# Kernel tuning notes

Hardware: AMD Instinct MI355X
Metric: run time of the kernel (lower is better)

The kernel has to match this reference:

```python
import jax, jax.numpy as jnp
import numpy as np

NODELEN = 394
N_NODES = 50000
N_EDGES = 200000
IN_DIM = 2 * NODELEN  # 788
H2 = 192
EMB = 128


def setup_inputs() -> dict:
    key = jax.random.key(0)
    ks = jax.random.split(key, 12)
    inp = {
        'features': jax.random.normal(ks[0], (N_NODES, NODELEN), dtype=jnp.float32),
        'src': jax.random.randint(ks[1], (N_EDGES,), 0, N_NODES),
        'dst': jax.random.randint(ks[2], (N_EDGES,), 0, N_NODES),
        # AutoEncoder params (Linear weights stored as [in, out])
        'W_enc1': jax.random.normal(ks[3], (IN_DIM, H2), dtype=jnp.float32) / np.sqrt(IN_DIM),
        'b_enc1': jnp.zeros((H2,), dtype=jnp.float32),
        'W_enc3': jax.random.normal(ks[4], (H2, EMB), dtype=jnp.float32) / np.sqrt(H2),
        'b_enc3': jnp.zeros((EMB,), dtype=jnp.float32),
        'W_dec1': jax.random.normal(ks[5], (EMB, H2), dtype=jnp.float32) / np.sqrt(EMB),
        'b_dec1': jnp.zeros((H2,), dtype=jnp.float32),
        'W_dec3': jax.random.normal(ks[6], (H2, IN_DIM), dtype=jnp.float32) / np.sqrt(H2),
        'b_dec3': jnp.zeros((IN_DIM,), dtype=jnp.float32),
    }
    return inp


def _segment_mean(msgs, dst, inv_deg, n):
    # msgs: [E, F] gathered neighbor features; mean over incoming edges per node
    return jax.ops.segment_sum(msgs, dst, num_segments=n) * inv_deg


def reference(features, src, dst, W_enc1, b_enc1, W_enc3, b_enc3,
              W_dec1, b_dec1, W_dec3, b_dec3):
    n = features.shape[0]
    ones = jnp.ones(src.shape[0], dtype=features.dtype)
    deg = jax.ops.segment_sum(ones, dst, num_segments=n)
    # nodes with no neighbors fall back to the zero dummy vector (as in source)
    inv_deg = (1.0 / jnp.maximum(deg, 1.0))[:, None]

    # depth-1 aggregation: mean of raw neighbor features, then feat[0] := 0
    h1 = _segment_mean(features[src], dst, inv_deg, n)
    h1 = h1.at[:, 0].set(0.0)
    # depth-2 aggregation: mean of depth-1 aggregates of neighbors, feat[0] := 0
    h2 = _segment_mean(h1[src], dst, inv_deg, n)
    h2 = h2.at[:, 0].set(0.0)

    # concatenated embedding with positions 0 and NODELEN zeroed
    emb = jnp.concatenate([features, h2], axis=1)  # [N, 788]
    emb = emb.at[:, 0].set(0.0).at[:, NODELEN].set(0.0)

    # AutoEncoder forward (dropout is identity at inference)
    x = jax.nn.relu(emb @ W_enc1 + b_enc1)
    encoded = x @ W_enc3 + b_enc3
    y = jax.nn.relu(encoded @ W_dec1 + b_dec1)
    decoded = y @ W_dec3 + b_dec3
    return encoded, decoded, emb
```

## Files before the change

### kernel.cpp

```cpp
#include <hip/hip_runtime.h>
#include <hip/hip_bf16.h>

#define NODELEN 394
#define IN_DIM 788
#define H2DIM 192
#define EMBDIM 128
#define NCHUNK 197

typedef __attribute__((ext_vector_type(4))) float f32x4;
typedef __attribute__((ext_vector_type(8))) short bfrag;

static __device__ __forceinline__ unsigned short f2bf(float f) {
    union { float f; unsigned u; } v; v.f = f;
    unsigned r = v.u + 0x7FFFu + ((v.u >> 16) & 1u);
    return (unsigned short)(r >> 16);
}
static __device__ __forceinline__ float bf2f(unsigned short h) {
    union { unsigned u; float f; } v; v.u = ((unsigned)h) << 16;
    return v.f;
}


__global__ void count_deg(const int* __restrict__ dst, int* __restrict__ deg, int e) {
    int i = blockIdx.x * blockDim.x + threadIdx.x;
    if (i < e) atomicAdd(&deg[dst[i]], 1);
}

__global__ void block_sum(const int* __restrict__ deg, int* __restrict__ bsum, int n) {
    __shared__ int s[256];
    int t = threadIdx.x;
    int i = blockIdx.x * 256 + t;
    s[t] = (i < n) ? deg[i] : 0;
    __syncthreads();
    for (int d = 128; d > 0; d >>= 1) {
        if (t < d) s[t] += s[t + d];
        __syncthreads();
    }
    if (t == 0) bsum[blockIdx.x] = s[0];
}

__global__ void scan_bsums(int* bsum, int nb) {
    __shared__ int s[256];
    int t = threadIdx.x;
    int x0 = (t < nb) ? bsum[t] : 0;
    s[t] = x0;
    __syncthreads();
    for (int d = 1; d < 256; d <<= 1) {
        int u = (t >= d) ? s[t - d] : 0;
        __syncthreads();
        s[t] += u;
        __syncthreads();
    }
    if (t < nb) bsum[t] = s[t] - x0;
}

__global__ void block_scan(const int* __restrict__ deg, const int* __restrict__ boff,
                           int* __restrict__ rowstart, int* __restrict__ cursor,
                           float* __restrict__ inv, int n) {
    __shared__ int s[256];
    int t = threadIdx.x;
    int i = blockIdx.x * 256 + t;
    int x0 = (i < n) ? deg[i] : 0;
    s[t] = x0;
    __syncthreads();
    for (int d = 1; d < 256; d <<= 1) {
        int u = (t >= d) ? s[t - d] : 0;
        __syncthreads();
        s[t] += u;
        __syncthreads();
    }
    if (i < n) {
        int r = boff[blockIdx.x] + s[t] - x0;
        rowstart[i] = r;
        cursor[i] = r;
        inv[i] = 1.0f / fmaxf((float)x0, 1.0f);
    }
}

__global__ void fill_edges(const int* __restrict__ src, const int* __restrict__ dst,
                           int* __restrict__ cursor, int* __restrict__ elist, int e) {
    int i = blockIdx.x * blockDim.x + threadIdx.x;
    if (i < e) {
        int p = atomicAdd(&cursor[dst[i]], 1);
        elist[p] = src[i];
    }
}


__global__ __launch_bounds__(256) void gather1(
        const float* __restrict__ feat, const int* __restrict__ rowstart,
        const int* __restrict__ deg, const float* __restrict__ inv,
        const int* __restrict__ elist, unsigned short* __restrict__ h1) {
    const int node = blockIdx.x;
    const int c = threadIdx.x;
    if (c >= NCHUNK) return;
    const int beg = rowstart[node];
    const int dc = deg[node];
    const float s = inv[node];
    const size_t off = (size_t)c * 2;

    float ax = 0.f, ay = 0.f, bx = 0.f, by = 0.f;
    float cx = 0.f, cy = 0.f, dx = 0.f, dy = 0.f;
    int j = 0;
    for (; j + 3 < dc; j += 4) {
        int n0 = elist[beg + j], n1 = elist[beg + j + 1];
        int n2 = elist[beg + j + 2], n3 = elist[beg + j + 3];
        float2 v0 = *(const float2*)(feat + (size_t)n0 * NODELEN + off);
        float2 v1 = *(const float2*)(feat + (size_t)n1 * NODELEN + off);
        float2 v2 = *(const float2*)(feat + (size_t)n2 * NODELEN + off);
        float2 v3 = *(const float2*)(feat + (size_t)n3 * NODELEN + off);
        ax += v0.x; ay += v0.y; bx += v1.x; by += v1.y;
        cx += v2.x; cy += v2.y; dx += v3.x; dy += v3.y;
    }
    for (; j < dc; ++j) {
        int n0 = elist[beg + j];
        float2 v0 = *(const float2*)(feat + (size_t)n0 * NODELEN + off);
        ax += v0.x; ay += v0.y;
    }
    float fx = (ax + bx + cx + dx) * s;
    float fy = (ay + by + cy + dy) * s;
    if (c == 0) fx = 0.f;
    unsigned out = ((unsigned)f2bf(fy) << 16) | (unsigned)f2bf(fx);
    *(unsigned*)(h1 + (size_t)node * NODELEN + off) = out;
}

__global__ __launch_bounds__(256) void gather2_emb(
        const float* __restrict__ feat, const unsigned* __restrict__ h1,
        const int* __restrict__ rowstart, const int* __restrict__ deg,
        const float* __restrict__ inv, const int* __restrict__ elist,
        float* __restrict__ emb) {
    const int node = blockIdx.x;
    const int c = threadIdx.x;
    if (c >= NCHUNK) return;
    const int beg = rowstart[node];
    const int dc = deg[node];
    const float s = inv[node];

    float ax = 0.f, ay = 0.f, bx = 0.f, by = 0.f;
    float cx = 0.f, cy = 0.f, dx = 0.f, dy = 0.f;
    int j = 0;
    for (; j + 3 < dc; j += 4) {
        int n0 = elist[beg + j], n1 = elist[beg + j + 1];
        int n2 = elist[beg + j + 2], n3 = elist[beg + j + 3];
        unsigned u0 = h1[(size_t)n0 * NCHUNK + c];
        unsigned u1 = h1[(size_t)n1 * NCHUNK + c];
        unsigned u2 = h1[(size_t)n2 * NCHUNK + c];
        unsigned u3 = h1[(size_t)n3 * NCHUNK + c];
        ax += bf2f((unsigned short)u0); ay += bf2f((unsigned short)(u0 >> 16));
        bx += bf2f((unsigned short)u1); by += bf2f((unsigned short)(u1 >> 16));
        cx += bf2f((unsigned short)u2); cy += bf2f((unsigned short)(u2 >> 16));
        dx += bf2f((unsigned short)u3); dy += bf2f((unsigned short)(u3 >> 16));
    }
    for (; j < dc; ++j) {
        int n0 = elist[beg + j];
        unsigned u0 = h1[(size_t)n0 * NCHUNK + c];
        ax += bf2f((unsigned short)u0); ay += bf2f((unsigned short)(u0 >> 16));
    }
    float hx = (ax + bx + cx + dx) * s;
    float hy = (ay + by + cy + dy) * s;

    const float* fr = feat + (size_t)node * NODELEN;
    float* er = emb + (size_t)node * IN_DIM;
    float2 fv = *(const float2*)(fr + c * 2);
    if (c == 0) { fv.x = 0.f; hx = 0.f; }
    *(float2*)(er + c * 2) = fv;
    float2 hv; hv.x = hx; hv.y = hy;
    *(float2*)(er + NODELEN + c * 2) = hv;
}

__device__ __forceinline__ void tr_one(const float* W, unsigned short* Wt,
                                       int K, int N, int Kp, int idx) {
    int nrow = idx / Kp, k = idx - nrow * Kp;
    Wt[idx] = (k < K) ? f2bf(W[(size_t)k * N + nrow]) : (unsigned short)0;
}

#define T1E (192 * 800)
#define T2E (128 * 192)
#define T3E (192 * 128)
#define T4E (788 * 192)

__global__ void transpose_all(const float* __restrict__ W1, unsigned short* __restrict__ Wt1,
                              const float* __restrict__ W2, unsigned short* __restrict__ Wt2,
                              const float* __restrict__ W3, unsigned short* __restrict__ Wt3,
                              const float* __restrict__ W4, unsigned short* __restrict__ Wt4) {
    int idx = blockIdx.x * 256 + threadIdx.x;
    if (idx < T1E) { tr_one(W1, Wt1, IN_DIM, H2DIM, 800, idx); return; }
    idx -= T1E;
    if (idx < T2E) { tr_one(W2, Wt2, H2DIM, EMBDIM, 192, idx); return; }
    idx -= T2E;
    if (idx < T3E) { tr_one(W3, Wt3, EMBDIM, H2DIM, 128, idx); return; }
    idx -= T3E;
    if (idx < T4E) { tr_one(W4, Wt4, H2DIM, IN_DIM, 192, idx); return; }
}

static __device__ __forceinline__ int bs_addr(int r, int s) {
    return r * 32 + ((s ^ ((r >> 1) & 3)) << 3);
}
static __device__ __forceinline__ int xy_base(int r, int s) {
    int ph = (s & 24) | ((s ^ r) & 7);
    return r * 192 + (ph << 3);
}
static __device__ __forceinline__ int xy_addr_s(int r, int col) { return xy_base(r, col >> 3) + (col & 7); }

static __device__ __forceinline__ unsigned short f2bf_fast(float f) {
    __hip_bfloat16 h = __float2bfloat16(f);
    union { __hip_bfloat16 h; unsigned short u; } c; c.h = h; return c.u;
}

struct A8 { float4 a, b; };

static __device__ __forceinline__ void load_a(A8 out[2], const float* __restrict__ emb,
                                              int m0, int wm, int lr, int lk, int M, int kt) {
    int c = kt * 32 + lk * 8;
    #pragma unroll
    for (int i = 0; i < 2; ++i) {
        int gm = m0 + wm * 32 + i * 16 + lr;
        const float* rp = emb + (size_t)gm * IN_DIM;
        bool v = gm < M;
        if (v && c + 8 <= IN_DIM) {
            out[i].a = *(const float4*)(rp + c);
            out[i].b = *(const float4*)(rp + c + 4);
        } else {
            float t[8];
            #pragma unroll
            for (int q = 0; q < 8; ++q) t[q] = (v && c + q < IN_DIM) ? rp[c + q] : 0.f;
            out[i].a = make_float4(t[0], t[1], t[2], t[3]);
            out[i].b = make_float4(t[4], t[5], t[6], t[7]);
        }
    }
}

static __device__ __forceinline__ bfrag cvt_a(const A8& x) {
    union { unsigned short u[8]; bfrag v; } pk;
    pk.u[0] = f2bf_fast(x.a.x); pk.u[1] = f2bf_fast(x.a.y);
    pk.u[2] = f2bf_fast(x.a.z); pk.u[3] = f2bf_fast(x.a.w);
    pk.u[4] = f2bf_fast(x.b.x); pk.u[5] = f2bf_fast(x.b.y);
    pk.u[6] = f2bf_fast(x.b.z); pk.u[7] = f2bf_fast(x.b.w);
    return pk.v;
}

__global__ __launch_bounds__(256, 3) void mlp12(
    const float* __restrict__ emb,
    const unsigned short* __restrict__ Wt1,
    const unsigned short* __restrict__ Wt2,
    const float* __restrict__ b1, const float* __restrict__ b2,
    float* __restrict__ encoded, unsigned short* __restrict__ enc16, int M)
{
    __shared__ unsigned short XY[64 * 192];
    __shared__ unsigned short Bs[2][192 * 32];

    const int tid = threadIdx.x;
    const int wid = tid >> 6, l = tid & 63;
    const int wm = wid >> 1, wn = wid & 1;
    const int lr = l & 15, lk = l >> 4;
    const int m0 = blockIdx.x * 64;

    const int r0 = tid >> 2, s0 = tid & 3;
    const int r1 = (tid + 256) >> 2;
    const int r2 = (tid + 512) >> 2;
    const int bw0 = bs_addr(r0, s0);
    const int bw1 = bs_addr(r1, s0);
    const int bw2 = bs_addr(r2, s0);
    int brd6[6], brd4[4];
    #pragma unroll
    for (int j = 0; j < 6; ++j) brd6[j] = bs_addr(wn * 96 + j * 16 + lr, lk);
    #pragma unroll
    for (int j = 0; j < 4; ++j) brd4[j] = bs_addr(wn * 64 + j * 16 + lr, lk);

    {
        f32x4 acc[2][6];
        #pragma unroll
        for (int i = 0; i < 2; ++i)
            #pragma unroll
            for (int j = 0; j < 6; ++j) acc[i][j] = (f32x4){0.f, 0.f, 0.f, 0.f};

        A8 aC[2], aN[2];
        bfrag bC[3], bN[3];
        load_a(aC, emb, m0, wm, lr, lk, M, 0);
        bC[0] = *(const bfrag*)(Wt1 + (size_t)r0 * 800 + s0 * 8);
        bC[1] = *(const bfrag*)(Wt1 + (size_t)r1 * 800 + s0 * 8);
        bC[2] = *(const bfrag*)(Wt1 + (size_t)r2 * 800 + s0 * 8);

        #pragma unroll 5
        for (int kt = 0; kt < 25; ++kt) {
            unsigned short* B = Bs[kt & 1];
            *(bfrag*)&B[bw0] = bC[0];
            *(bfrag*)&B[bw1] = bC[1];
            *(bfrag*)&B[bw2] = bC[2];
            if (kt < 24) {
                int k0 = (kt + 1) * 32;
                load_a(aN, emb, m0, wm, lr, lk, M, kt + 1);
                bN[0] = *(const bfrag*)(Wt1 + (size_t)r0 * 800 + k0 + s0 * 8);
                bN[1] = *(const bfrag*)(Wt1 + (size_t)r1 * 800 + k0 + s0 * 8);
                bN[2] = *(const bfrag*)(Wt1 + (size_t)r2 * 800 + k0 + s0 * 8);
            }
            __syncthreads();
            bfrag af0 = cvt_a(aC[0]), af1 = cvt_a(aC[1]);
            bfrag bf[6];
            #pragma unroll
            for (int j = 0; j < 6; ++j) bf[j] = *(const bfrag*)&B[brd6[j]];
            #pragma unroll
            for (int j = 0; j < 6; ++j) {
                acc[0][j] = __builtin_amdgcn_mfma_f32_16x16x32_bf16(af0, bf[j], acc[0][j], 0, 0, 0);
                acc[1][j] = __builtin_amdgcn_mfma_f32_16x16x32_bf16(af1, bf[j], acc[1][j], 0, 0, 0);
            }
            if (kt < 24) {
                aC[0] = aN[0]; aC[1] = aN[1];
                bC[0] = bN[0]; bC[1] = bN[1]; bC[2] = bN[2];
            }
        }
        float bv[6];
        #pragma unroll
        for (int j = 0; j < 6; ++j) bv[j] = b1[wn * 96 + j * 16 + lr];
        #pragma unroll
        for (int i = 0; i < 2; ++i)
            #pragma unroll
            for (int j = 0; j < 6; ++j)
                #pragma unroll
                for (int r = 0; r < 4; ++r) {
                    int m = wm * 32 + i * 16 + lk * 4 + r;
                    int n1 = wn * 96 + j * 16 + lr;
                    XY[xy_addr_s(m, n1)] = f2bf_fast(fmaxf(acc[i][j][r] + bv[j], 0.f));
                }
    }
    __syncthreads();

    {
        bfrag af2[6][2];
        #pragma unroll
        for (int q = 0; q < 6; ++q)
            #pragma unroll
            for (int i = 0; i < 2; ++i)
                af2[q][i] = *(const bfrag*)&XY[xy_base(wm * 32 + i * 16 + lr, q * 4 + lk)];

        f32x4 acc[2][4];
        #pragma unroll
        for (int i = 0; i < 2; ++i)
            #pragma unroll
            for (int j = 0; j < 4; ++j) acc[i][j] = (f32x4){0.f, 0.f, 0.f, 0.f};

        bfrag bC[2], bN[2];
        bC[0] = *(const bfrag*)(Wt2 + (size_t)r0 * 192 + s0 * 8);
        bC[1] = *(const bfrag*)(Wt2 + (size_t)r1 * 192 + s0 * 8);

        #pragma unroll
        for (int kt = 0; kt < 6; ++kt) {
            unsigned short* B = Bs[kt & 1];
            *(bfrag*)&B[bw0] = bC[0];
            *(bfrag*)&B[bw1] = bC[1];
            if (kt < 5) {
                int k0 = (kt + 1) * 32;
                bN[0] = *(const bfrag*)(Wt2 + (size_t)r0 * 192 + k0 + s0 * 8);
                bN[1] = *(const bfrag*)(Wt2 + (size_t)r1 * 192 + k0 + s0 * 8);
            }
            __syncthreads();
            bfrag bf[4];
            #pragma unroll
            for (int j = 0; j < 4; ++j) bf[j] = *(const bfrag*)&B[brd4[j]];
            #pragma unroll
            for (int i = 0; i < 2; ++i)
                #pragma unroll
                for (int j = 0; j < 4; ++j)
                    acc[i][j] = __builtin_amdgcn_mfma_f32_16x16x32_bf16(af2[kt][i], bf[j], acc[i][j], 0, 0, 0);
            if (kt < 5) { bC[0] = bN[0]; bC[1] = bN[1]; }
        }

        float bv[4];
        #pragma unroll
        for (int j = 0; j < 4; ++j) bv[j] = b2[wn * 64 + j * 16 + lr];
        #pragma unroll
        for (int i = 0; i < 2; ++i)
            #pragma unroll
            for (int j = 0; j < 4; ++j)
                #pragma unroll
                for (int r = 0; r < 4; ++r) {
                    int m = wm * 32 + i * 16 + lk * 4 + r;
                    int nn = wn * 64 + j * 16 + lr;
                    float v = acc[i][j][r] + bv[j];
                    int gm = m0 + m;
                    if (gm < M) {
                        encoded[(size_t)gm * EMBDIM + nn] = v;
                        enc16[(size_t)gm * EMBDIM + nn] = f2bf_fast(v);
                    }
                }
    }
}

__global__ __launch_bounds__(256, 3) void mlp34(
    const unsigned short* __restrict__ enc16,
    const unsigned short* __restrict__ Wt3,
    const unsigned short* __restrict__ Wt4,
    const float* __restrict__ b3, const float* __restrict__ b4,
    float* __restrict__ decoded, int M)
{
    __shared__ unsigned short XY[64 * 192];
    __shared__ unsigned short Bs[2][192 * 32];

    const int tid = threadIdx.x;
    const int wid = tid >> 6, l = tid & 63;
    const int wm = wid >> 1, wn = wid & 1;
    const int lr = l & 15, lk = l >> 4;
    const int m0 = blockIdx.x * 64;
    const bfrag zf = {0, 0, 0, 0, 0, 0, 0, 0};

    const int r0 = tid >> 2, s0 = tid & 3;
    const int r1 = (tid + 256) >> 2;
    const int r2 = (tid + 512) >> 2;
    const int bw0 = bs_addr(r0, s0);
    const int bw1 = bs_addr(r1, s0);
    const int bw2 = bs_addr(r2, s0);
    int brd6[6];
    #pragma unroll
    for (int j = 0; j < 6; ++j) brd6[j] = bs_addr(wn * 96 + j * 16 + lr, lk);

    {
        bfrag af3[4][2];
        #pragma unroll
        for (int q = 0; q < 4; ++q)
            #pragma unroll
            for (int i = 0; i < 2; ++i) {
                int gm = m0 + wm * 32 + i * 16 + lr;
                af3[q][i] = (gm < M)
                    ? *(const bfrag*)(enc16 + (size_t)gm * EMBDIM + q * 32 + lk * 8) : zf;
            }

        f32x4 acc[2][6];
        #pragma unroll
        for (int i = 0; i < 2; ++i)
            #pragma unroll
            for (int j = 0; j < 6; ++j) acc[i][j] = (f32x4){0.f, 0.f, 0.f, 0.f};

        bfrag bC[3], bN[3];
        bC[0] = *(const bfrag*)(Wt3 + (size_t)r0 * 128 + s0 * 8);
        bC[1] = *(const bfrag*)(Wt3 + (size_t)r1 * 128 + s0 * 8);
        bC[2] = *(const bfrag*)(Wt3 + (size_t)r2 * 128 + s0 * 8);

        #pragma unroll
        for (int kt = 0; kt < 4; ++kt) {
            unsigned short* B = Bs[kt & 1];
            *(bfrag*)&B[bw0] = bC[0];
            *(bfrag*)&B[bw1] = bC[1];
            *(bfrag*)&B[bw2] = bC[2];
            if (kt < 3) {
                int k0 = (kt + 1) * 32;
                bN[0] = *(const bfrag*)(Wt3 + (size_t)r0 * 128 + k0 + s0 * 8);
                bN[1] = *(const bfrag*)(Wt3 + (size_t)r1 * 128 + k0 + s0 * 8);
                bN[2] = *(const bfrag*)(Wt3 + (size_t)r2 * 128 + k0 + s0 * 8);
            }
            __syncthreads();
            bfrag bf[6];
            #pragma unroll
            for (int j = 0; j < 6; ++j) bf[j] = *(const bfrag*)&B[brd6[j]];
            #pragma unroll
            for (int i = 0; i < 2; ++i)
                #pragma unroll
                for (int j = 0; j < 6; ++j)
                    acc[i][j] = __builtin_amdgcn_mfma_f32_16x16x32_bf16(af3[kt][i], bf[j], acc[i][j], 0, 0, 0);
            if (kt < 3) { bC[0] = bN[0]; bC[1] = bN[1]; bC[2] = bN[2]; }
        }

        float bv[6];
        #pragma unroll
        for (int j = 0; j < 6; ++j) bv[j] = b3[wn * 96 + j * 16 + lr];
        #pragma unroll
        for (int i = 0; i < 2; ++i)
            #pragma unroll
            for (int j = 0; j < 6; ++j)
                #pragma unroll
                for (int r = 0; r < 4; ++r) {
                    int m = wm * 32 + i * 16 + lk * 4 + r;
                    int nc = wn * 96 + j * 16 + lr;
                    XY[xy_addr_s(m, nc)] = f2bf_fast(fmaxf(acc[i][j][r] + bv[j], 0.f));
                }
    }
    __syncthreads();

    {
        bfrag af4[6][2];
        #pragma unroll
        for (int q = 0; q < 6; ++q)
            #pragma unroll
            for (int i = 0; i < 2; ++i)
                af4[q][i] = *(const bfrag*)&XY[xy_base(wm * 32 + i * 16 + lr, q * 4 + lk)];

        bfrag bC[3], bN[3];
        bC[0] = *(const bfrag*)(Wt4 + (size_t)r0 * 192 + s0 * 8);
        bC[1] = *(const bfrag*)(Wt4 + (size_t)r1 * 192 + s0 * 8);
        bC[2] = *(const bfrag*)(Wt4 + (size_t)r2 * 192 + s0 * 8);

        for (int nc = 0; nc < 5; ++nc) {
            f32x4 acc[2][6];
            #pragma unroll
            for (int i = 0; i < 2; ++i)
                #pragma unroll
                for (int j = 0; j < 6; ++j) acc[i][j] = (f32x4){0.f, 0.f, 0.f, 0.f};

            #pragma unroll
            for (int kt = 0; kt < 6; ++kt) {
                const int t = nc * 6 + kt;
                unsigned short* B = Bs[t & 1];
                *(bfrag*)&B[bw0] = bC[0];
                *(bfrag*)&B[bw1] = bC[1];
                *(bfrag*)&B[bw2] = bC[2];
                if (t < 29) {
                    int nn = (kt < 5) ? nc : nc + 1;
                    int nk = (kt < 5) ? (kt + 1) * 32 : 0;
                    int g0 = nn * 192 + r0, g1 = nn * 192 + r1, g2 = nn * 192 + r2;
                    bN[0] = (g0 < IN_DIM) ? *(const bfrag*)(Wt4 + (size_t)g0 * 192 + nk + s0 * 8) : zf;
                    bN[1] = (g1 < IN_DIM) ? *(const bfrag*)(Wt4 + (size_t)g1 * 192 + nk + s0 * 8) : zf;
                    bN[2] = (g2 < IN_DIM) ? *(const bfrag*)(Wt4 + (size_t)g2 * 192 + nk + s0 * 8) : zf;
                }
                __syncthreads();
                bfrag bf[6];
                #pragma unroll
                for (int j = 0; j < 6; ++j) bf[j] = *(const bfrag*)&B[brd6[j]];
                #pragma unroll
                for (int i = 0; i < 2; ++i)
                    #pragma unroll
                    for (int j = 0; j < 6; ++j)
                        acc[i][j] = __builtin_amdgcn_mfma_f32_16x16x32_bf16(af4[kt][i], bf[j], acc[i][j], 0, 0, 0);
                bC[0] = bN[0]; bC[1] = bN[1]; bC[2] = bN[2];
            }

            float bv[6];
            #pragma unroll
            for (int j = 0; j < 6; ++j) {
                int nn = nc * 192 + wn * 96 + j * 16 + lr;
                bv[j] = (nn < IN_DIM) ? b4[nn] : 0.f;
            }
            #pragma unroll
            for (int i = 0; i < 2; ++i)
                #pragma unroll
                for (int j = 0; j < 6; ++j)
                    #pragma unroll
                    for (int r = 0; r < 4; ++r) {
                        int gm = m0 + wm * 32 + i * 16 + lk * 4 + r;
                        int nn = nc * 192 + wn * 96 + j * 16 + lr;
                        if (gm < M && nn < IN_DIM)
                            decoded[(size_t)gm * IN_DIM + nn] = acc[i][j][r] + bv[j];
                    }
        }
    }
}


extern "C" void kernel_launch(void* const* d_in, const int* in_sizes, int n_in,
                              void* d_out, int out_size, void* d_ws, size_t ws_size,
                              hipStream_t stream) {
    const float* features = (const float*)d_in[0];
    const int*   src      = (const int*)d_in[1];
    const int*   dst      = (const int*)d_in[2];
    const float* W_enc1   = (const float*)d_in[3];
    const float* b_enc1   = (const float*)d_in[4];
    const float* W_enc3   = (const float*)d_in[5];
    const float* b_enc3   = (const float*)d_in[6];
    const float* W_dec1   = (const float*)d_in[7];
    const float* b_dec1   = (const float*)d_in[8];
    const float* W_dec3   = (const float*)d_in[9];
    const float* b_dec3   = (const float*)d_in[10];

    const int n = in_sizes[0] / NODELEN;
    const int e = in_sizes[1];

    float* encoded = (float*)d_out;
    float* decoded = encoded + (size_t)n * EMBDIM;
    float* emb     = decoded + (size_t)n * IN_DIM;

    char* ws = (char*)d_ws;
    unsigned short* h1    = (unsigned short*)(ws + 0);
    unsigned short* enc16 = (unsigned short*)(ws + 0);
    unsigned short* Wt1 = (unsigned short*)(ws + 40000000);
    unsigned short* Wt2 = (unsigned short*)(ws + 40400000);
    unsigned short* Wt3 = (unsigned short*)(ws + 40500000);
    unsigned short* Wt4 = (unsigned short*)(ws + 40600000);
    float* inv          = (float*)(ws + 41000000);
    int*   deg          = (int*)  (ws + 41200000);
    int*   rowstart     = (int*)  (ws + 41400000);
    int*   cursor       = (int*)  (ws + 41600000);
    int*   elist        = (int*)  (ws + 41800000);
    int*   bsum         = (int*)  (ws + 42600000);

    const int nb = (n + 255) / 256;
    const int eb = (e + 255) / 256;

    transpose_all<<<(T1E + T2E + T3E + T4E + 255) / 256, 256, 0, stream>>>(
        W_enc1, Wt1, W_enc3, Wt2, W_dec1, Wt3, W_dec3, Wt4);

    hipMemsetAsync(deg, 0, (size_t)n * sizeof(int), stream);
    count_deg<<<eb, 256, 0, stream>>>(dst, deg, e);
    block_sum<<<nb, 256, 0, stream>>>(deg, bsum, n);
    scan_bsums<<<1, 256, 0, stream>>>(bsum, nb);
    block_scan<<<nb, 256, 0, stream>>>(deg, bsum, rowstart, cursor, inv, n);
    fill_edges<<<eb, 256, 0, stream>>>(src, dst, cursor, elist, e);

    gather1<<<n, 256, 0, stream>>>(features, rowstart, deg, inv, elist, h1);
    gather2_emb<<<n, 256, 0, stream>>>(features, (const unsigned*)h1, rowstart, deg,
                                       inv, elist, emb);

    const int MB = (n + 63) / 64;
    mlp12<<<MB, 256, 0, stream>>>(emb, Wt1, Wt2, b_enc1, b_enc3, encoded, enc16, n);
    mlp34<<<MB, 256, 0, stream>>>(enc16, Wt3, Wt4, b_dec1, b_dec3, decoded, n);
}
```

Before: 350.7 us.

## Enlarge MLP row tiles to 128 and stage a bf16 copy of emb

Both MLP kernels now give each block 128 rows instead of 64, so each weight tile loaded into shared memory feeds more MFMAs. Occupancy drops to 2 blocks per CU. The double-buffered B pipeline now writes the next buffer after the MFMAs with a single barrier per step, and the decoder uses 128-column N tiles. When the workspace is large enough, gather2 also writes a padded bf16 copy of emb, so mlp12 reads half as many bytes and skips the fp32-to-bf16 conversion. The cost is an extra write pass and more register pressure.

```diff
diff --git a/kernel.cpp b/kernel.cpp
--- a/kernel.cpp
+++ b/kernel.cpp
@@ -10,6 +10,9 @@
 typedef __attribute__((ext_vector_type(4))) float f32x4;
 typedef __attribute__((ext_vector_type(8))) short bfrag;
 
+#define LBAR() do { asm volatile("s_waitcnt lgkmcnt(0)" ::: "memory"); \
+                    __builtin_amdgcn_s_barrier(); } while (0)
+
 static __device__ __forceinline__ unsigned short f2bf(float f) {
     union { float f; unsigned u; } v; v.f = f;
     unsigned r = v.u + 0x7FFFu + ((v.u >> 16) & 1u);
@@ -18,6 +21,10 @@
 static __device__ __forceinline__ float bf2f(unsigned short h) {
     union { unsigned u; float f; } v; v.u = ((unsigned)h) << 16;
     return v.f;
+}
+static __device__ __forceinline__ unsigned short f2bf_fast(float f) {
+    __hip_bfloat16 h = __float2bfloat16(f);
+    union { __hip_bfloat16 h; unsigned short u; } c; c.h = h; return c.u;
 }
 
 
@@ -128,7 +135,7 @@
         const float* __restrict__ feat, const unsigned* __restrict__ h1,
         const int* __restrict__ rowstart, const int* __restrict__ deg,
         const float* __restrict__ inv, const int* __restrict__ elist,
-        float* __restrict__ emb) {
+        float* __restrict__ emb, unsigned* __restrict__ emb16u) {
     const int node = blockIdx.x;
     const int c = threadIdx.x;
     if (c >= NCHUNK) return;
@@ -166,6 +173,13 @@
     *(float2*)(er + c * 2) = fv;
     float2 hv; hv.x = hx; hv.y = hy;
     *(float2*)(er + NODELEN + c * 2) = hv;
+
+    if (emb16u) {
+        unsigned* e16 = emb16u + (size_t)node * 400;
+        e16[c]          = ((unsigned)f2bf(fv.y) << 16) | (unsigned)f2bf(fv.x);
+        e16[NCHUNK + c] = ((unsigned)f2bf(hy)  << 16) | (unsigned)f2bf(hx);
+        if (c < 6) e16[394 + c] = 0u;
+    }
 }
 
 __device__ __forceinline__ void tr_one(const float* W, unsigned short* Wt,
@@ -202,62 +216,50 @@
 }
 static __device__ __forceinline__ int xy_addr_s(int r, int col) { return xy_base(r, col >> 3) + (col & 7); }
 
-static __device__ __forceinline__ unsigned short f2bf_fast(float f) {
-    __hip_bfloat16 h = __float2bfloat16(f);
-    union { __hip_bfloat16 h; unsigned short u; } c; c.h = h; return c.u;
-}
-
-struct A8 { float4 a, b; };
-
-static __device__ __forceinline__ void load_a(A8 out[2], const float* __restrict__ emb,
-                                              int m0, int wm, int lr, int lk, int M, int kt) {
-    int c = kt * 32 + lk * 8;
-    #pragma unroll
-    for (int i = 0; i < 2; ++i) {
-        int gm = m0 + wm * 32 + i * 16 + lr;
-        const float* rp = emb + (size_t)gm * IN_DIM;
-        bool v = gm < M;
-        if (v && c + 8 <= IN_DIM) {
-            out[i].a = *(const float4*)(rp + c);
-            out[i].b = *(const float4*)(rp + c + 4);
+static __device__ __forceinline__ bfrag load_af_bf(const unsigned short* A800, int gm, int M, int col) {
+    const bfrag zf = {0, 0, 0, 0, 0, 0, 0, 0};
+    return (gm < M) ? *(const bfrag*)(A800 + (size_t)gm * 800 + col) : zf;
+}
+static __device__ __forceinline__ bfrag load_af_f32(const float* A, int gm, int M, int col) {
+    float t[8];
+    #pragma unroll
+    for (int q = 0; q < 8; ++q) t[q] = 0.f;
+    if (gm < M) {
+        const float* rp = A + (size_t)gm * IN_DIM;
+        if (col + 8 <= IN_DIM) {
+            float4 v0 = *(const float4*)(rp + col), v1 = *(const float4*)(rp + col + 4);
+            t[0] = v0.x; t[1] = v0.y; t[2] = v0.z; t[3] = v0.w;
+            t[4] = v1.x; t[5] = v1.y; t[6] = v1.z; t[7] = v1.w;
         } else {
-            float t[8];
-            #pragma unroll
-            for (int q = 0; q < 8; ++q) t[q] = (v && c + q < IN_DIM) ? rp[c + q] : 0.f;
-            out[i].a = make_float4(t[0], t[1], t[2], t[3]);
-            out[i].b = make_float4(t[4], t[5], t[6], t[7]);
+            #pragma unroll
+            for (int q = 0; q < 8; ++q) if (col + q < IN_DIM) t[q] = rp[col + q];
         }
     }
-}
-
-static __device__ __forceinline__ bfrag cvt_a(const A8& x) {
     union { unsigned short u[8]; bfrag v; } pk;
-    pk.u[0] = f2bf_fast(x.a.x); pk.u[1] = f2bf_fast(x.a.y);
-    pk.u[2] = f2bf_fast(x.a.z); pk.u[3] = f2bf_fast(x.a.w);
-    pk.u[4] = f2bf_fast(x.b.x); pk.u[5] = f2bf_fast(x.b.y);
-    pk.u[6] = f2bf_fast(x.b.z); pk.u[7] = f2bf_fast(x.b.w);
+    #pragma unroll
+    for (int q = 0; q < 8; ++q) pk.u[q] = f2bf_fast(t[q]);
     return pk.v;
 }
 
-__global__ __launch_bounds__(256, 3) void mlp12(
-    const float* __restrict__ emb,
+template <int ABF>
+__global__ __launch_bounds__(256, 2) void mlp12(
+    const void* __restrict__ Aemb,
     const unsigned short* __restrict__ Wt1,
     const unsigned short* __restrict__ Wt2,
     const float* __restrict__ b1, const float* __restrict__ b2,
     float* __restrict__ encoded, unsigned short* __restrict__ enc16, int M)
 {
-    __shared__ unsigned short XY[64 * 192];
+    __shared__ unsigned short XY[128 * 192];
     __shared__ unsigned short Bs[2][192 * 32];
 
     const int tid = threadIdx.x;
     const int wid = tid >> 6, l = tid & 63;
     const int wm = wid >> 1, wn = wid & 1;
     const int lr = l & 15, lk = l >> 4;
-    const int m0 = blockIdx.x * 64;
+    const int m0 = blockIdx.x * 128;
 
     const int r0 = tid >> 2, s0 = tid & 3;
-    const int r1 = (tid + 256) >> 2;
-    const int r2 = (tid + 512) >> 2;
+    const int r1 = r0 + 64, r2 = r0 + 128;
     const int bw0 = bs_addr(r0, s0);
     const int bw1 = bs_addr(r1, s0);
     const int bw2 = bs_addr(r2, s0);
@@ -267,58 +269,68 @@
     #pragma unroll
     for (int j = 0; j < 4; ++j) brd4[j] = bs_addr(wn * 64 + j * 16 + lr, lk);
 
+    int gmA[4];
+    #pragma unroll
+    for (int i = 0; i < 4; ++i) gmA[i] = m0 + wm * 64 + i * 16 + lr;
+
     {
-        f32x4 acc[2][6];
-        #pragma unroll
-        for (int i = 0; i < 2; ++i)
+        f32x4 acc[4][6];
+        #pragma unroll
+        for (int i = 0; i < 4; ++i)
             #pragma unroll
             for (int j = 0; j < 6; ++j) acc[i][j] = (f32x4){0.f, 0.f, 0.f, 0.f};
 
-        A8 aC[2], aN[2];
-        bfrag bC[3], bN[3];
-        load_a(aC, emb, m0, wm, lr, lk, M, 0);
-        bC[0] = *(const bfrag*)(Wt1 + (size_t)r0 * 800 + s0 * 8);
-        bC[1] = *(const bfrag*)(Wt1 + (size_t)r1 * 800 + s0 * 8);
-        bC[2] = *(const bfrag*)(Wt1 + (size_t)r2 * 800 + s0 * 8);
+        bfrag afC[4], afN[4], bN[3];
+        #pragma unroll
+        for (int i = 0; i < 4; ++i)
+            afC[i] = ABF ? load_af_bf((const unsigned short*)Aemb, gmA[i], M, lk * 8)
+                         : load_af_f32((const float*)Aemb, gmA[i], M, lk * 8);
+        *(bfrag*)&Bs[0][bw0] = *(const bfrag*)(Wt1 + (size_t)r0 * 800 + s0 * 8);
+        *(bfrag*)&Bs[0][bw1] = *(const bfrag*)(Wt1 + (size_t)r1 * 800 + s0 * 8);
+        *(bfrag*)&Bs[0][bw2] = *(const bfrag*)(Wt1 + (size_t)r2 * 800 + s0 * 8);
+        LBAR();
 
         #pragma unroll 5
         for (int kt = 0; kt < 25; ++kt) {
-            unsigned short* B = Bs[kt & 1];
-            *(bfrag*)&B[bw0] = bC[0];
-            *(bfrag*)&B[bw1] = bC[1];
-            *(bfrag*)&B[bw2] = bC[2];
             if (kt < 24) {
                 int k0 = (kt + 1) * 32;
-                load_a(aN, emb, m0, wm, lr, lk, M, kt + 1);
+                #pragma unroll
+                for (int i = 0; i < 4; ++i)
+                    afN[i] = ABF ? load_af_bf((const unsigned short*)Aemb, gmA[i], M, k0 + lk * 8)
+                                 : load_af_f32((const float*)Aemb, gmA[i], M, k0 + lk * 8);
                 bN[0] = *(const bfrag*)(Wt1 + (size_t)r0 * 800 + k0 + s0 * 8);
                 bN[1] = *(const bfrag*)(Wt1 + (size_t)r1 * 800 + k0 + s0 * 8);
                 bN[2] = *(const bfrag*)(Wt1 + (size_t)r2 * 800 + k0 + s0 * 8);
             }
-            __syncthreads();
-            bfrag af0 = cvt_a(aC[0]), af1 = cvt_a(aC[1]);
+            const unsigned short* B = Bs[kt & 1];
             bfrag bf[6];
             #pragma unroll
             for (int j = 0; j < 6; ++j) bf[j] = *(const bfrag*)&B[brd6[j]];
             #pragma unroll
-            for (int j = 0; j < 6; ++j) {
-                acc[0][j] = __builtin_amdgcn_mfma_f32_16x16x32_bf16(af0, bf[j], acc[0][j], 0, 0, 0);
-                acc[1][j] = __builtin_amdgcn_mfma_f32_16x16x32_bf16(af1, bf[j], acc[1][j], 0, 0, 0);
-            }
+            for (int i = 0; i < 4; ++i)
+                #pragma unroll
+                for (int j = 0; j < 6; ++j)
+                    acc[i][j] = __builtin_amdgcn_mfma_f32_16x16x32_bf16(afC[i], bf[j], acc[i][j], 0, 0, 0);
             if (kt < 24) {
-                aC[0] = aN[0]; aC[1] = aN[1];
-                bC[0] = bN[0]; bC[1] = bN[1]; bC[2] = bN[2];
+                unsigned short* Bn = Bs[(kt + 1) & 1];
+                *(bfrag*)&Bn[bw0] = bN[0];
+                *(bfrag*)&Bn[bw1] = bN[1];
+                *(bfrag*)&Bn[bw2] = bN[2];
+                LBAR();
+                #pragma unroll
+                for (int i = 0; i < 4; ++i) afC[i] = afN[i];
             }
         }
         float bv[6];
         #pragma unroll
         for (int j = 0; j < 6; ++j) bv[j] = b1[wn * 96 + j * 16 + lr];
         #pragma unroll
-        for (int i = 0; i < 2; ++i)
+        for (int i = 0; i < 4; ++i)
             #pragma unroll
             for (int j = 0; j < 6; ++j)
                 #pragma unroll
                 for (int r = 0; r < 4; ++r) {
-                    int m = wm * 32 + i * 16 + lk * 4 + r;
+                    int m = wm * 64 + i * 16 + lk * 4 + r;
                     int n1 = wn * 96 + j * 16 + lr;
                     XY[xy_addr_s(m, n1)] = f2bf_fast(fmaxf(acc[i][j][r] + bv[j], 0.f));
                 }
@@ -326,55 +338,54 @@
     __syncthreads();
 
     {
-        bfrag af2[6][2];
-        #pragma unroll
-        for (int q = 0; q < 6; ++q)
-            #pragma unroll
-            for (int i = 0; i < 2; ++i)
-                af2[q][i] = *(const bfrag*)&XY[xy_base(wm * 32 + i * 16 + lr, q * 4 + lk)];
-
-        f32x4 acc[2][4];
-        #pragma unroll
-        for (int i = 0; i < 2; ++i)
+        f32x4 acc[4][4];
+        #pragma unroll
+        for (int i = 0; i < 4; ++i)
             #pragma unroll
             for (int j = 0; j < 4; ++j) acc[i][j] = (f32x4){0.f, 0.f, 0.f, 0.f};
 
-        bfrag bC[2], bN[2];
-        bC[0] = *(const bfrag*)(Wt2 + (size_t)r0 * 192 + s0 * 8);
-        bC[1] = *(const bfrag*)(Wt2 + (size_t)r1 * 192 + s0 * 8);
+        bfrag bN[2];
+        *(bfrag*)&Bs[0][bw0] = *(const bfrag*)(Wt2 + (size_t)r0 * 192 + s0 * 8);
+        *(bfrag*)&Bs[0][bw1] = *(const bfrag*)(Wt2 + (size_t)r1 * 192 + s0 * 8);
+        LBAR();
 
         #pragma unroll
         for (int kt = 0; kt < 6; ++kt) {
-            unsigned short* B = Bs[kt & 1];
-            *(bfrag*)&B[bw0] = bC[0];
-            *(bfrag*)&B[bw1] = bC[1];
             if (kt < 5) {
                 int k0 = (kt + 1) * 32;
                 bN[0] = *(const bfrag*)(Wt2 + (size_t)r0 * 192 + k0 + s0 * 8);
                 bN[1] = *(const bfrag*)(Wt2 + (size_t)r1 * 192 + k0 + s0 * 8);
             }
-            __syncthreads();
-            bfrag bf[4];
+            const unsigned short* B = Bs[kt & 1];
+            bfrag af[4], bf[4];
+            #pragma unroll
+            for (int i = 0; i < 4; ++i)
+                af[i] = *(const bfrag*)&XY[xy_base(wm * 64 + i * 16 + lr, kt * 4 + lk)];
             #pragma unroll
             for (int j = 0; j < 4; ++j) bf[j] = *(const bfrag*)&B[brd4[j]];
             #pragma unroll
-            for (int i = 0; i < 2; ++i)
+            for (int i = 0; i < 4; ++i)
                 #pragma unroll
                 for (int j = 0; j < 4; ++j)
-                    acc[i][j] = __builtin_amdgcn_mfma_f32_16x16x32_bf16(af2[kt][i], bf[j], acc[i][j], 0, 0, 0);
-            if (kt < 5) { bC[0] = bN[0]; bC[1] = bN[1]; }
+                    acc[i][j] = __builtin_amdgcn_mfma_f32_16x16x32_bf16(af[i], bf[j], acc[i][j], 0, 0, 0);
+            if (kt < 5) {
+                unsigned short* Bn = Bs[(kt + 1) & 1];
+                *(bfrag*)&Bn[bw0] = bN[0];
+                *(bfrag*)&Bn[bw1] = bN[1];
+                LBAR();
+            }
         }
 
         float bv[4];
         #pragma unroll
         for (int j = 0; j < 4; ++j) bv[j] = b2[wn * 64 + j * 16 + lr];
         #pragma unroll
-        for (int i = 0; i < 2; ++i)
+        for (int i = 0; i < 4; ++i)
             #pragma unroll
             for (int j = 0; j < 4; ++j)
                 #pragma unroll
                 for (int r = 0; r < 4; ++r) {
-                    int m = wm * 32 + i * 16 + lk * 4 + r;
+                    int m = wm * 64 + i * 16 + lk * 4 + r;
                     int nn = wn * 64 + j * 16 + lr;
                     float v = acc[i][j][r] + bv[j];
                     int gm = m0 + m;
@@ -386,89 +397,96 @@
     }
 }
 
-__global__ __launch_bounds__(256, 3) void mlp34(
+__global__ __launch_bounds__(256, 2) void mlp34(
     const unsigned short* __restrict__ enc16,
     const unsigned short* __restrict__ Wt3,
     const unsigned short* __restrict__ Wt4,
     const float* __restrict__ b3, const float* __restrict__ b4,
     float* __restrict__ decoded, int M)
 {
-    __shared__ unsigned short XY[64 * 192];
+    __shared__ unsigned short XY[128 * 192];
     __shared__ unsigned short Bs[2][192 * 32];
 
     const int tid = threadIdx.x;
     const int wid = tid >> 6, l = tid & 63;
     const int wm = wid >> 1, wn = wid & 1;
     const int lr = l & 15, lk = l >> 4;
-    const int m0 = blockIdx.x * 64;
+    const int m0 = blockIdx.x * 128;
     const bfrag zf = {0, 0, 0, 0, 0, 0, 0, 0};
 
     const int r0 = tid >> 2, s0 = tid & 3;
-    const int r1 = (tid + 256) >> 2;
-    const int r2 = (tid + 512) >> 2;
+    const int r1 = r0 + 64, r2 = r0 + 128;
     const int bw0 = bs_addr(r0, s0);
     const int bw1 = bs_addr(r1, s0);
     const int bw2 = bs_addr(r2, s0);
-    int brd6[6];
+    int brd6[6], brd4[4];
     #pragma unroll
     for (int j = 0; j < 6; ++j) brd6[j] = bs_addr(wn * 96 + j * 16 + lr, lk);
+    #pragma unroll
+    for (int j = 0; j < 4; ++j) brd4[j] = bs_addr(wn * 64 + j * 16 + lr, lk);
+
+    int gmA[4];
+    #pragma unroll
+    for (int i = 0; i < 4; ++i) gmA[i] = m0 + wm * 64 + i * 16 + lr;
 
     {
-        bfrag af3[4][2];
-        #pragma unroll
-        for (int q = 0; q < 4; ++q)
-            #pragma unroll
-            for (int i = 0; i < 2; ++i) {
-                int gm = m0 + wm * 32 + i * 16 + lr;
-                af3[q][i] = (gm < M)
-                    ? *(const bfrag*)(enc16 + (size_t)gm * EMBDIM + q * 32 + lk * 8) : zf;
-            }
-
-        f32x4 acc[2][6];
-        #pragma unroll
-        for (int i = 0; i < 2; ++i)
+        f32x4 acc[4][6];
+        #pragma unroll
+        for (int i = 0; i < 4; ++i)
             #pragma unroll
             for (int j = 0; j < 6; ++j) acc[i][j] = (f32x4){0.f, 0.f, 0.f, 0.f};
 
-        bfrag bC[3], bN[3];
-        bC[0] = *(const bfrag*)(Wt3 + (size_t)r0 * 128 + s0 * 8);
-        bC[1] = *(const bfrag*)(Wt3 + (size_t)r1 * 128 + s0 * 8);
-        bC[2] = *(const bfrag*)(Wt3 + (size_t)r2 * 128 + s0 * 8);
+        bfrag afC[4], afN[4], bN[3];
+        #pragma unroll
+        for (int i = 0; i < 4; ++i)
+            afC[i] = (gmA[i] < M) ? *(const bfrag*)(enc16 + (size_t)gmA[i] * EMBDIM + lk * 8) : zf;
+        *(bfrag*)&Bs[0][bw0] = *(const bfrag*)(Wt3 + (size_t)r0 * 128 + s0 * 8);
+        *(bfrag*)&Bs[0][bw1] = *(const bfrag*)(Wt3 + (size_t)r1 * 128 + s0 * 8);
+        *(bfrag*)&Bs[0][bw2] = *(const bfrag*)(Wt3 + (size_t)r2 * 128 + s0 * 8);
+        LBAR();
 
         #pragma unroll
         for (int kt = 0; kt < 4; ++kt) {
-            unsigned short* B = Bs[kt & 1];
-            *(bfrag*)&B[bw0] = bC[0];
-            *(bfrag*)&B[bw1] = bC[1];
-            *(bfrag*)&B[bw2] = bC[2];
             if (kt < 3) {
                 int k0 = (kt + 1) * 32;
+                #pragma unroll
+                for (int i = 0; i < 4; ++i)
+                    afN[i] = (gmA[i] < M)
+                        ? *(const bfrag*)(enc16 + (size_t)gmA[i] * EMBDIM + k0 + lk * 8) : zf;
                 bN[0] = *(const bfrag*)(Wt3 + (size_t)r0 * 128 + k0 + s0 * 8);
                 bN[1] = *(const bfrag*)(Wt3 + (size_t)r1 * 128 + k0 + s0 * 8);
                 bN[2] = *(const bfrag*)(Wt3 + (size_t)r2 * 128 + k0 + s0 * 8);
             }
-            __syncthreads();
+            const unsigned short* B = Bs[kt & 1];
             bfrag bf[6];
             #pragma unroll
             for (int j = 0; j < 6; ++j) bf[j] = *(const bfrag*)&B[brd6[j]];
             #pragma unroll
-            for (int i = 0; i < 2; ++i)
+            for (int i = 0; i < 4; ++i)
                 #pragma unroll
                 for (int j = 0; j < 6; ++j)
-                    acc[i][j] = __builtin_amdgcn_mfma_f32_16x16x32_bf16(af3[kt][i], bf[j], acc[i][j], 0, 0, 0);
-            if (kt < 3) { bC[0] = bN[0]; bC[1] = bN[1]; bC[2] = bN[2]; }
+                    acc[i][j] = __builtin_amdgcn_mfma_f32_16x16x32_bf16(afC[i], bf[j], acc[i][j], 0, 0, 0);
+            if (kt < 3) {
+                unsigned short* Bn = Bs[(kt + 1) & 1];
+                *(bfrag*)&Bn[bw0] = bN[0];
+                *(bfrag*)&Bn[bw1] = bN[1];
+                *(bfrag*)&Bn[bw2] = bN[2];
+                LBAR();
+                #pragma unroll
+                for (int i = 0; i < 4; ++i) afC[i] = afN[i];
+            }
         }
 
         float bv[6];
         #pragma unroll
         for (int j = 0; j < 6; ++j) bv[j] = b3[wn * 96 + j * 16 + lr];
         #pragma unroll
-        for (int i = 0; i < 2; ++i)
+        for (int i = 0; i < 4; ++i)
             #pragma unroll
             for (int j = 0; j < 6; ++j)
                 #pragma unroll
                 for (int r = 0; r < 4; ++r) {
-                    int m = wm * 32 + i * 16 + lk * 4 + r;
+                    int m = wm * 64 + i * 16 + lk * 4 + r;
                     int nc = wn * 96 + j * 16 + lr;
                     XY[xy_addr_s(m, nc)] = f2bf_fast(fmaxf(acc[i][j][r] + bv[j], 0.f));
                 }
@@ -476,66 +494,66 @@
     __syncthreads();
 
     {
-        bfrag af4[6][2];
+        bfrag af4[6][4];
         #pragma unroll
         for (int q = 0; q < 6; ++q)
             #pragma unroll
-            for (int i = 0; i < 2; ++i)
-                af4[q][i] = *(const bfrag*)&XY[xy_base(wm * 32 + i * 16 + lr, q * 4 + lk)];
-
-        bfrag bC[3], bN[3];
-        bC[0] = *(const bfrag*)(Wt4 + (size_t)r0 * 192 + s0 * 8);
-        bC[1] = *(const bfrag*)(Wt4 + (size_t)r1 * 192 + s0 * 8);
-        bC[2] = *(const bfrag*)(Wt4 + (size_t)r2 * 192 + s0 * 8);
-
-        for (int nc = 0; nc < 5; ++nc) {
-            f32x4 acc[2][6];
-            #pragma unroll
-            for (int i = 0; i < 2; ++i)
-                #pragma unroll
-                for (int j = 0; j < 6; ++j) acc[i][j] = (f32x4){0.f, 0.f, 0.f, 0.f};
+            for (int i = 0; i < 4; ++i)
+                af4[q][i] = *(const bfrag*)&XY[xy_base(wm * 64 + i * 16 + lr, q * 4 + lk)];
+
+        bfrag bN[2];
+        *(bfrag*)&Bs[0][bw0] = *(const bfrag*)(Wt4 + (size_t)r0 * 192 + s0 * 8);
+        *(bfrag*)&Bs[0][bw1] = *(const bfrag*)(Wt4 + (size_t)r1 * 192 + s0 * 8);
+        LBAR();
+
+        for (int nc = 0; nc < 7; ++nc) {
+            f32x4 acc[4][4];
+            #pragma unroll
+            for (int i = 0; i < 4; ++i)
+                #pragma unroll
+                for (int j = 0; j < 4; ++j) acc[i][j] = (f32x4){0.f, 0.f, 0.f, 0.f};
 
             #pragma unroll
             for (int kt = 0; kt < 6; ++kt) {
-                const int t = nc * 6 + kt;
-                unsigned short* B = Bs[t & 1];
-                *(bfrag*)&B[bw0] = bC[0];
-                *(bfrag*)&B[bw1] = bC[1];
-                *(bfrag*)&B[bw2] = bC[2];
-                if (t < 29) {
+                const bool last = (nc == 6) && (kt == 5);
+                if (!last) {
                     int nn = (kt < 5) ? nc : nc + 1;
                     int nk = (kt < 5) ? (kt + 1) * 32 : 0;
-                    int g0 = nn * 192 + r0, g1 = nn * 192 + r1, g2 = nn * 192 + r2;
+                    int g0 = nn * 128 + r0, g1 = nn * 128 + r1;
                     bN[0] = (g0 < IN_DIM) ? *(const bfrag*)(Wt4 + (size_t)g0 * 192 + nk + s0 * 8) : zf;
                     bN[1] = (g1 < IN_DIM) ? *(const bfrag*)(Wt4 + (size_t)g1 * 192 + nk + s0 * 8) : zf;
-                    bN[2] = (g2 < IN_DIM) ? *(const bfrag*)(Wt4 + (size_t)g2 * 192 + nk + s0 * 8) : zf;
                 }
-                __syncthreads();
-                bfrag bf[6];
-                #pragma unroll
-                for (int j = 0; j < 6; ++j) bf[j] = *(const bfrag*)&B[brd6[j]];
-                #pragma unroll
-                for (int i = 0; i < 2; ++i)
+                const unsigned short* B = Bs[kt & 1];
+                bfrag bf[4];
+                #pragma unroll
+                for (int j = 0; j < 4; ++j) bf[j] = *(const bfrag*)&B[brd4[j]];
+                #pragma unroll
+                for (int i = 0; i < 4; ++i)
                     #pragma unroll
-                    for (int j = 0; j < 6; ++j)
+                    for (int j = 0; j < 4; ++j)
                         acc[i][j] = __builtin_amdgcn_mfma_f32_16x16x32_bf16(af4[kt][i], bf[j], acc[i][j], 0, 0, 0);
-                bC[0] = bN[0]; bC[1] = bN[1]; bC[2] = bN[2];
-            }
-
-            float bv[6];
-            #pragma unroll
-            for (int j = 0; j < 6; ++j) {
-                int nn = nc * 192 + wn * 96 + j * 16 + lr;
+                if (!last) {
+                    unsigned short* Bn = Bs[(kt + 1) & 1];
+                    *(bfrag*)&Bn[bw0] = bN[0];
+                    *(bfrag*)&Bn[bw1] = bN[1];
+                    LBAR();
+                }
+            }
+
+            float bv[4];
+            #pragma unroll
+            for (int j = 0; j < 4; ++j) {
+                int nn = nc * 128 + wn * 64 + j * 16 + lr;
                 bv[j] = (nn < IN_DIM) ? b4[nn] : 0.f;
             }
             #pragma unroll
-            for (int i = 0; i < 2; ++i)
-                #pragma unroll
-                for (int j = 0; j < 6; ++j)
+            for (int i = 0; i < 4; ++i)
+                #pragma unroll
+                for (int j = 0; j < 4; ++j)
                     #pragma unroll
                     for (int r = 0; r < 4; ++r) {
-                        int gm = m0 + wm * 32 + i * 16 + lk * 4 + r;
-                        int nn = nc * 192 + wn * 96 + j * 16 + lr;
+                        int gm = m0 + wm * 64 + i * 16 + lk * 4 + r;
+                        int nn = nc * 128 + wn * 64 + j * 16 + lr;
                         if (gm < M && nn < IN_DIM)
                             decoded[(size_t)gm * IN_DIM + nn] = acc[i][j][r] + bv[j];
                     }
@@ -579,6 +597,9 @@
     int*   cursor       = (int*)  (ws + 41600000);
     int*   elist        = (int*)  (ws + 41800000);
     int*   bsum         = (int*)  (ws + 42600000);
+    unsigned short* emb16 = (unsigned short*)(ws + 44000000);
+    const size_t NEED = 44000000ull + (size_t)n * 800 * 2;
+    const int useBF = (ws_size >= NEED) ? 1 : 0;
 
     const int nb = (n + 255) / 256;
     const int eb = (e + 255) / 256;
@@ -595,9 +616,14 @@
 
     gather1<<<n, 256, 0, stream>>>(features, rowstart, deg, inv, elist, h1);
     gather2_emb<<<n, 256, 0, stream>>>(features, (const unsigned*)h1, rowstart, deg,
-                                       inv, elist, emb);
-
-    const int MB = (n + 63) / 64;
-    mlp12<<<MB, 256, 0, stream>>>(emb, Wt1, Wt2, b_enc1, b_enc3, encoded, enc16, n);
+                                       inv, elist, emb,
+                                       useBF ? (unsigned*)emb16 : nullptr);
+
+    const int MB = (n + 127) / 128;
+    if (useBF) {
+        mlp12<1><<<MB, 256, 0, stream>>>(emb16, Wt1, Wt2, b_enc1, b_enc3, encoded, enc16, n);
+    } else {
+        mlp12<0><<<MB, 256, 0, stream>>>(emb, Wt1, Wt2, b_enc1, b_enc3, encoded, enc16, n);
+    }
     mlp34<<<MB, 256, 0, stream>>>(enc16, Wt3, Wt4, b_dec1, b_dec3, decoded, n);
 }
```

After: 341.1 us. -2.7%, faster.
